# Kernel optimization log

Measured on AMD Instinct MI355X. Metric: run time of the kernel, lower is better.

## Reference

```python
import jax, jax.numpy as jnp
import numpy as np

TEMP_LP = 0.05  # args.temp_lp_loss


def setup_inputs() -> dict:
    key = jax.random.key(0)
    k1, k2, k3, k4 = jax.random.split(key, 4)
    B, B_s, topk, C, n_ids = 4096, 4096, 4, 128, 751
    feats = jax.random.normal(k1, (B, C), dtype=jnp.float32)
    feats_s = jax.random.normal(k2, (B_s, topk, C), dtype=jnp.float32)
    labels = jax.random.randint(k3, (B,), 0, n_ids)
    labels_s = jax.random.randint(k4, (B_s * topk,), 0, n_ids)
    return {"feats": feats, "feats_s": feats_s, "labels": labels, "labels_s": labels_s}


def reference(feats, feats_s, labels, labels_s):
    # feats: [B, C]; feats_s: [B_s, topk, C] -> [N, C] with N = B_s*topk
    B, C = feats.shape
    fs = feats_s.reshape(-1, C)
    sim = (feats @ fs.T) / TEMP_LP                      # [B, N]
    # Per-sample: target puts weight 1/P on the P positives (labels_s == label),
    # 0 on negatives. Concatenation order does not affect log_softmax values, so
    # loss_i = -(1/P) * sum_{j in pos} (sim[i,j] - logsumexp(sim[i,:]))
    lse = jax.nn.logsumexpsim = None
    lse = jax.nn.logsumexp(sim, axis=1)                 # [B]
    pos = labels[:, None] == labels_s[None, :]          # [B, N] bool
    P = pos.sum(axis=1).astype(sim.dtype)               # [B]
    pos_sum = jnp.sum(jnp.where(pos, sim, jnp.zeros((), sim.dtype)), axis=1)
    loss_i = lse - pos_sum / P                          # [B]
    return jnp.sum(loss_i) / B
```

## Files before the change

kernel.cpp:

```cpp
#include <hip/hip_runtime.h>
#include <hip/hip_bf16.h>

#define B_ROWS 4096
#define N_COLS 16384
#define CDIM   128
#define NIDS   751
#define TEMP_INV 20.0f
#define ASCALE 28.853900817779268f
#define LN2 0.6931471805599453f

#define BM 256
#define BN 64
#define NCHUNK 32
#define COLS_PER_CHUNK (N_COLS / NCHUNK)
#define STEPS (COLS_PER_CHUNK / BN)
#define LSE_BLOCKS ((B_ROWS / BM) * NCHUNK)
#define POS_BLOCKS (N_COLS / 256)

typedef __attribute__((ext_vector_type(8))) short short8;
typedef __attribute__((ext_vector_type(4))) float f32x4;
typedef __attribute__((ext_vector_type(4))) unsigned short u16x4;

#define AS1 __attribute__((address_space(1)))
#define AS3 __attribute__((address_space(3)))

__device__ __forceinline__ unsigned short f2bf(float x) {
  union { float f; unsigned u; } c; c.f = x;
  unsigned r = c.u + 0x7FFFu + ((c.u >> 16) & 1u);
  return (unsigned short)(r >> 16);
}

__global__ void prep_kernel(const float* __restrict__ feats, const float* __restrict__ fs,
                            const int* __restrict__ labels, const int* __restrict__ labels_s,
                            unsigned short* __restrict__ feats_bf, unsigned short* __restrict__ fs_bf,
                            float* __restrict__ Ftab, float* __restrict__ Pcnt) {
  const int bid = blockIdx.x;
  const int NF4 = B_ROWS * CDIM / 4;
  const int NCVT_BLK = (NF4 + N_COLS * CDIM / 4) / 256;
  if (bid < NCVT_BLK) {
    int idx = bid * 256 + threadIdx.x;
    if (idx < NF4) {
      f32x4 v = ((const f32x4*)feats)[idx];
      u16x4 o = { f2bf(v[0] * ASCALE), f2bf(v[1] * ASCALE), f2bf(v[2] * ASCALE), f2bf(v[3] * ASCALE) };
      ((u16x4*)feats_bf)[idx] = o;
    } else {
      int j = idx - NF4;
      f32x4 v = ((const f32x4*)fs)[j];
      u16x4 o = { f2bf(v[0]), f2bf(v[1]), f2bf(v[2]), f2bf(v[3]) };
      ((u16x4*)fs_bf)[j] = o;
    }
  } else if (bid < NCVT_BLK + (B_ROWS * CDIM) / 256) {
    int idx = (bid - NCVT_BLK) * 256 + threadIdx.x;
    int row = idx >> 7, c = idx & 127;
    atomicAdd(&Ftab[labels[row] * CDIM + c], feats[idx]);
  } else {
    int j = (bid - NCVT_BLK - (B_ROWS * CDIM) / 256) * 256 + threadIdx.x;
    atomicAdd(&Pcnt[labels_s[j]], 1.0f);
  }
}

__launch_bounds__(256, 2)
__global__ void main_kernel(const unsigned short* __restrict__ A,
                            const unsigned short* __restrict__ Bm,
                            const float* __restrict__ fs32,
                            const int* __restrict__ labels_s,
                            const float* __restrict__ Ftab, const float* __restrict__ Pcnt,
                            float* __restrict__ pm, float* __restrict__ ps,
                            float* __restrict__ acc) {
  __shared__ unsigned short lds[2][BN * CDIM];
  __shared__ float wsum[4];

  if (blockIdx.x >= LSE_BLOCKS) {
    int j = (blockIdx.x - LSE_BLOCKS) * 256 + threadIdx.x;
    int l = labels_s[j];
    const f32x4* fr = (const f32x4*)(fs32 + (size_t)j * CDIM);
    const f32x4* Fr = (const f32x4*)(Ftab + (size_t)l * CDIM);
    float d = 0.f;
#pragma unroll
    for (int q = 0; q < CDIM / 4; ++q) {
      f32x4 a = fr[q], b = Fr[q];
      d += a[0] * b[0] + a[1] * b[1] + a[2] * b[2] + a[3] * b[3];
    }
    d /= Pcnt[l];
#pragma unroll
    for (int off = 1; off < 64; off <<= 1) d += __shfl_xor(d, off, 64);
    if ((threadIdx.x & 63) == 0) wsum[threadIdx.x >> 6] = d;
    __syncthreads();
    if (threadIdx.x == 0) atomicAdd(&acc[1], wsum[0] + wsum[1] + wsum[2] + wsum[3]);
    return;
  }

  const int tid = threadIdx.x, wv = tid >> 6, ln = tid & 63;
  const int hi = ln >> 4, lo = ln & 15;
  const int ch = blockIdx.x & (NCHUNK - 1);
  const int rb = blockIdx.x >> 5;
  const int col_base = ch * COLS_PER_CHUNK;

  const unsigned short* aptr = A + (size_t)(rb * BM + wv * 64 + lo) * CDIM + hi * 8;
  short8 afr[4][4];
#pragma unroll
  for (int rg = 0; rg < 4; ++rg)
#pragma unroll
    for (int kk = 0; kk < 4; ++kk)
      afr[rg][kk] = *(const short8*)(aptr + rg * 16 * CDIM + kk * 32);

  float m_[4][4], s_[4][4];
#pragma unroll
  for (int rg = 0; rg < 4; ++rg)
#pragma unroll
    for (int j = 0; j < 4; ++j) { m_[rg][j] = -1e30f; s_[rg][j] = 0.f; }

  auto stage = [&](int buf, int step) {
    const int c0 = col_base + step * BN;
    char* base = (char*)&lds[buf][0];
#pragma unroll
    for (int r = 0; r < 4; ++r) {
      int q = r * 256 + wv * 64 + ln;
      int row = q >> 4, cc = q & 15;
      int cs = cc ^ (row & 7);
      const unsigned short* src = Bm + (size_t)(c0 + row) * CDIM + cs * 8;
      __builtin_amdgcn_global_load_lds((AS1 const void*)src,
                                       (AS3 void*)(base + (size_t)(r * 256 + wv * 64) * 16),
                                       16, 0, 0);
    }
  };

  stage(0, 0);
  int cur = 0;
  for (int t = 0; t < STEPS; ++t) {
    if (t + 1 < STEPS) {
      stage(cur ^ 1, t + 1);
      asm volatile("s_waitcnt vmcnt(4)" ::: "memory");
    } else {
      asm volatile("s_waitcnt vmcnt(0)" ::: "memory");
    }
    __builtin_amdgcn_s_barrier();
    __builtin_amdgcn_sched_barrier(0);

    f32x4 accv[4][4];
#pragma unroll
    for (int ct = 0; ct < 4; ++ct) {
      const int rowT = ct * 16 + lo;
      short8 bf[4];
#pragma unroll
      for (int kk = 0; kk < 4; ++kk) {
        int q = kk * 4 + hi;
        int qs = q ^ (rowT & 7);
        bf[kk] = *(const short8*)&lds[cur][rowT * CDIM + qs * 8];
      }
#pragma unroll
      for (int rg = 0; rg < 4; ++rg) {
        f32x4 c4 = {0.f, 0.f, 0.f, 0.f};
#pragma unroll
        for (int kk = 0; kk < 4; ++kk)
          c4 = __builtin_amdgcn_mfma_f32_16x16x32_bf16(afr[rg][kk], bf[kk], c4, 0, 0, 0);
        accv[rg][ct] = c4;
      }
    }

#pragma unroll
    for (int rg = 0; rg < 4; ++rg)
#pragma unroll
      for (int j = 0; j < 4; ++j) {
        float v0 = accv[rg][0][j], v1 = accv[rg][1][j];
        float v2 = accv[rg][2][j], v3 = accv[rg][3][j];
        float mx = fmaxf(fmaxf(v0, v1), fmaxf(v2, v3));
        float mn = fmaxf(m_[rg][j], mx);
        s_[rg][j] = s_[rg][j] * __builtin_amdgcn_exp2f(m_[rg][j] - mn)
                  + (__builtin_amdgcn_exp2f(v0 - mn) + __builtin_amdgcn_exp2f(v1 - mn))
                  + (__builtin_amdgcn_exp2f(v2 - mn) + __builtin_amdgcn_exp2f(v3 - mn));
        m_[rg][j] = mn;
      }

    __builtin_amdgcn_sched_barrier(0);
    __builtin_amdgcn_s_barrier();
    cur ^= 1;
  }

#pragma unroll
  for (int rg = 0; rg < 4; ++rg)
#pragma unroll
    for (int j = 0; j < 4; ++j) {
#pragma unroll
      for (int off = 1; off < 16; off <<= 1) {
        float mo = __shfl_xor(m_[rg][j], off, 64);
        float so = __shfl_xor(s_[rg][j], off, 64);
        float mn = fmaxf(m_[rg][j], mo);
        s_[rg][j] = s_[rg][j] * __builtin_amdgcn_exp2f(m_[rg][j] - mn)
                  + so * __builtin_amdgcn_exp2f(mo - mn);
        m_[rg][j] = mn;
      }
    }

  if (lo == 0) {
    int rbase = rb * BM + wv * 64;
#pragma unroll
    for (int rg = 0; rg < 4; ++rg)
#pragma unroll
      for (int j = 0; j < 4; ++j) {
        int row = rbase + rg * 16 + hi * 4 + j;
        pm[(size_t)ch * B_ROWS + row] = m_[rg][j];
        ps[(size_t)ch * B_ROWS + row] = s_[rg][j];
      }
  }
}

__global__ void combine_kernel(const float* __restrict__ pm, const float* __restrict__ ps,
                               float* __restrict__ acc, float* __restrict__ out) {
  int row = blockIdx.x * blockDim.x + threadIdx.x;
  float mg = -1e30f, sg = 0.f;
#pragma unroll
  for (int c = 0; c < NCHUNK; ++c) {
    float mp = pm[c * B_ROWS + row], sp = ps[c * B_ROWS + row];
    float mn = fmaxf(mg, mp);
    sg = sg * __builtin_amdgcn_exp2f(mg - mn) + sp * __builtin_amdgcn_exp2f(mp - mn);
    mg = mn;
  }
  float lse = LN2 * mg + logf(sg);
#pragma unroll
  for (int off = 1; off < 64; off <<= 1) lse += __shfl_xor(lse, off, 64);
  __shared__ float wsum[4];
  if ((threadIdx.x & 63) == 0) wsum[threadIdx.x >> 6] = lse;
  __syncthreads();
  if (threadIdx.x == 0) {
    atomicAdd(&acc[0], wsum[0] + wsum[1] + wsum[2] + wsum[3]);
    __threadfence();
    unsigned old = atomicAdd((unsigned*)&acc[2], 1u);
    if (old == (B_ROWS / 256) - 1) {
      float a0 = atomicAdd(&acc[0], 0.f);
      float a1 = atomicAdd(&acc[1], 0.f);
      out[0] = (a0 - TEMP_INV * a1) * (1.0f / (float)B_ROWS);
    }
  }
}

extern "C" void kernel_launch(void* const* d_in, const int* in_sizes, int n_in,
                              void* d_out, int out_size, void* d_ws, size_t ws_size,
                              hipStream_t stream) {
  const float* feats   = (const float*)d_in[0];
  const float* feats_s = (const float*)d_in[1];
  const int* labels    = (const int*)d_in[2];
  const int* labels_s  = (const int*)d_in[3];
  float* out = (float*)d_out;

  char* ws = (char*)d_ws;
  size_t off = 0;
  auto carve = [&](size_t bytes) -> char* {
    char* p = ws + off;
    off += (bytes + 255) & ~(size_t)255;
    return p;
  };
  unsigned short* feats_bf = (unsigned short*)carve((size_t)B_ROWS * CDIM * 2);
  unsigned short* fs_bf    = (unsigned short*)carve((size_t)N_COLS * CDIM * 2);
  size_t zstart = off;
  float* Ftab = (float*)carve((size_t)NIDS * CDIM * 4);
  float* Pcnt = (float*)carve((size_t)NIDS * 4);
  float* acc  = (float*)carve(4 * 4);
  size_t zend = off;
  float* pm   = (float*)carve((size_t)NCHUNK * B_ROWS * 4);
  float* ps   = (float*)carve((size_t)NCHUNK * B_ROWS * 4);

  hipMemsetAsync(ws + zstart, 0, zend - zstart, stream);

  const int NPREP = (B_ROWS * CDIM / 4 + N_COLS * CDIM / 4) / 256
                  + (B_ROWS * CDIM) / 256
                  + N_COLS / 256;
  prep_kernel<<<NPREP, 256, 0, stream>>>(feats, feats_s, labels, labels_s,
                                         feats_bf, fs_bf, Ftab, Pcnt);
  main_kernel<<<LSE_BLOCKS + POS_BLOCKS, 256, 0, stream>>>(feats_bf, fs_bf, feats_s, labels_s,
                                                           Ftab, Pcnt, pm, ps, acc);
  combine_kernel<<<B_ROWS / 256, 256, 0, stream>>>(pm, ps, acc, out);
}
```

Measured before the change: 112.7 us.

## Replace global-atomic scatter with per-label LDS tables, drop memset, fuse partial LSE

Class-sum and count tables are now built by per-16-label blocks that each scan the labels, gather matching rows into a shared list and accumulate them with shared-memory atomics. This replaces global float atomics and removes the separate memset launch, since the tables are fully written and acc is zeroed inside prep. The main kernel now writes a single log2-sum per chunk instead of separate max and sum arrays, which halves partial traffic and simplifies the combine. The LDS swizzle is widened to 16. The rewritten prep rescans all labels in every table block, and the list is capped at 2048 entries per 16 labels; a larger group would silently drop rows.

Measured after the change: 148.6 us. 31.9% more time.

```diff
diff --git a/kernel.cpp b/kernel.cpp
--- a/kernel.cpp
+++ b/kernel.cpp
@@ -16,6 +16,7 @@
 #define STEPS (COLS_PER_CHUNK / BN)
 #define LSE_BLOCKS ((B_ROWS / BM) * NCHUNK)
 #define POS_BLOCKS (N_COLS / 256)
+#define NTBL ((NIDS + 15) / 16)
 
 typedef __attribute__((ext_vector_type(8))) short short8;
 typedef __attribute__((ext_vector_type(4))) float f32x4;
@@ -33,12 +34,48 @@
 __global__ void prep_kernel(const float* __restrict__ feats, const float* __restrict__ fs,
                             const int* __restrict__ labels, const int* __restrict__ labels_s,
                             unsigned short* __restrict__ feats_bf, unsigned short* __restrict__ fs_bf,
-                            float* __restrict__ Ftab, float* __restrict__ Pcnt) {
+                            float* __restrict__ Ftab, float* __restrict__ Pcnt,
+                            float* __restrict__ acc) {
   const int bid = blockIdx.x;
-  const int NF4 = B_ROWS * CDIM / 4;
-  const int NCVT_BLK = (NF4 + N_COLS * CDIM / 4) / 256;
-  if (bid < NCVT_BLK) {
-    int idx = bid * 256 + threadIdx.x;
+  const int tid = threadIdx.x;
+  if (bid < NTBL) {
+    __shared__ float Facc[16 * CDIM];
+    __shared__ int   list[2048];
+    __shared__ float Pc[16];
+    __shared__ int   cnt;
+    const int lo_l = bid * 16;
+    if (bid == 0 && tid < 4) acc[tid] = 0.f;
+    for (int i = tid; i < 16 * CDIM; i += 256) Facc[i] = 0.f;
+    if (tid < 16) Pc[tid] = 0.f;
+    if (tid == 0) cnt = 0;
+    __syncthreads();
+    for (int r = tid; r < B_ROWS; r += 256) {
+      unsigned d = (unsigned)(labels[r] - lo_l);
+      if (d < 16u) {
+        int k = atomicAdd(&cnt, 1);
+        if (k < 2048) list[k] = (r << 4) | (int)d;
+      }
+    }
+    for (int r = tid; r < N_COLS; r += 256) {
+      unsigned d = (unsigned)(labels_s[r] - lo_l);
+      if (d < 16u) atomicAdd(&Pc[d], 1.0f);
+    }
+    __syncthreads();
+    int n = min(cnt, 2048);
+    int c = tid & 127;
+    for (int k = tid >> 7; k < n; k += 2) {
+      int e = list[k]; int r = e >> 4, ll = e & 15;
+      atomicAdd(&Facc[ll * CDIM + c], feats[(size_t)r * CDIM + c]);
+    }
+    __syncthreads();
+    for (int i = tid; i < 16 * CDIM; i += 256) {
+      int gl = lo_l + (i >> 7);
+      if (gl < NIDS) Ftab[(size_t)gl * CDIM + (i & 127)] = Facc[i];
+    }
+    if (tid < 16 && lo_l + tid < NIDS) Pcnt[lo_l + tid] = Pc[tid];
+  } else {
+    const int NF4 = B_ROWS * CDIM / 4;
+    int idx = (bid - NTBL) * 256 + tid;
     if (idx < NF4) {
       f32x4 v = ((const f32x4*)feats)[idx];
       u16x4 o = { f2bf(v[0] * ASCALE), f2bf(v[1] * ASCALE), f2bf(v[2] * ASCALE), f2bf(v[3] * ASCALE) };
@@ -49,13 +86,6 @@
       u16x4 o = { f2bf(v[0]), f2bf(v[1]), f2bf(v[2]), f2bf(v[3]) };
       ((u16x4*)fs_bf)[j] = o;
     }
-  } else if (bid < NCVT_BLK + (B_ROWS * CDIM) / 256) {
-    int idx = (bid - NCVT_BLK) * 256 + threadIdx.x;
-    int row = idx >> 7, c = idx & 127;
-    atomicAdd(&Ftab[labels[row] * CDIM + c], feats[idx]);
-  } else {
-    int j = (bid - NCVT_BLK - (B_ROWS * CDIM) / 256) * 256 + threadIdx.x;
-    atomicAdd(&Pcnt[labels_s[j]], 1.0f);
   }
 }
 
@@ -65,13 +95,14 @@
                             const float* __restrict__ fs32,
                             const int* __restrict__ labels_s,
                             const float* __restrict__ Ftab, const float* __restrict__ Pcnt,
-                            float* __restrict__ pm, float* __restrict__ ps,
+                            float* __restrict__ pmL,
                             float* __restrict__ acc) {
   __shared__ unsigned short lds[2][BN * CDIM];
   __shared__ float wsum[4];
+  const int tid = threadIdx.x;
 
   if (blockIdx.x >= LSE_BLOCKS) {
-    int j = (blockIdx.x - LSE_BLOCKS) * 256 + threadIdx.x;
+    int j = (blockIdx.x - LSE_BLOCKS) * 256 + tid;
     int l = labels_s[j];
     const f32x4* fr = (const f32x4*)(fs32 + (size_t)j * CDIM);
     const f32x4* Fr = (const f32x4*)(Ftab + (size_t)l * CDIM);
@@ -84,13 +115,13 @@
     d /= Pcnt[l];
 #pragma unroll
     for (int off = 1; off < 64; off <<= 1) d += __shfl_xor(d, off, 64);
-    if ((threadIdx.x & 63) == 0) wsum[threadIdx.x >> 6] = d;
-    __syncthreads();
-    if (threadIdx.x == 0) atomicAdd(&acc[1], wsum[0] + wsum[1] + wsum[2] + wsum[3]);
+    if ((tid & 63) == 0) wsum[tid >> 6] = d;
+    __syncthreads();
+    if (tid == 0) atomicAdd(&acc[1], wsum[0] + wsum[1] + wsum[2] + wsum[3]);
     return;
   }
 
-  const int tid = threadIdx.x, wv = tid >> 6, ln = tid & 63;
+  const int wv = tid >> 6, ln = tid & 63;
   const int hi = ln >> 4, lo = ln & 15;
   const int ch = blockIdx.x & (NCHUNK - 1);
   const int rb = blockIdx.x >> 5;
@@ -117,7 +148,7 @@
     for (int r = 0; r < 4; ++r) {
       int q = r * 256 + wv * 64 + ln;
       int row = q >> 4, cc = q & 15;
-      int cs = cc ^ (row & 7);
+      int cs = cc ^ (row & 15);
       const unsigned short* src = Bm + (size_t)(c0 + row) * CDIM + cs * 8;
       __builtin_amdgcn_global_load_lds((AS1 const void*)src,
                                        (AS3 void*)(base + (size_t)(r * 256 + wv * 64) * 16),
@@ -144,8 +175,7 @@
       short8 bf[4];
 #pragma unroll
       for (int kk = 0; kk < 4; ++kk) {
-        int q = kk * 4 + hi;
-        int qs = q ^ (rowT & 7);
+        int qs = (kk * 4 + hi) ^ (rowT & 15);
         bf[kk] = *(const short8*)&lds[cur][rowT * CDIM + qs * 8];
       }
 #pragma unroll
@@ -193,29 +223,31 @@
     }
 
   if (lo == 0) {
-    int rbase = rb * BM + wv * 64;
+    int rbase = rb * BM + wv * 64 + hi * 4;
 #pragma unroll
     for (int rg = 0; rg < 4; ++rg)
 #pragma unroll
       for (int j = 0; j < 4; ++j) {
-        int row = rbase + rg * 16 + hi * 4 + j;
-        pm[(size_t)ch * B_ROWS + row] = m_[rg][j];
-        ps[(size_t)ch * B_ROWS + row] = s_[rg][j];
-      }
-  }
-}
-
-__global__ void combine_kernel(const float* __restrict__ pm, const float* __restrict__ ps,
-                               float* __restrict__ acc, float* __restrict__ out) {
+        int row = rbase + rg * 16 + j;
+        pmL[(size_t)ch * B_ROWS + row] = m_[rg][j] + __log2f(s_[rg][j]);
+      }
+  }
+}
+
+__global__ void combine_kernel(const float* __restrict__ pmL,
+                               float* __restrict__ acc,
+                               float* __restrict__ out) {
   int row = blockIdx.x * blockDim.x + threadIdx.x;
-  float mg = -1e30f, sg = 0.f;
+  float L[NCHUNK];
+  float mg = -1e30f;
 #pragma unroll
   for (int c = 0; c < NCHUNK; ++c) {
-    float mp = pm[c * B_ROWS + row], sp = ps[c * B_ROWS + row];
-    float mn = fmaxf(mg, mp);
-    sg = sg * __builtin_amdgcn_exp2f(mg - mn) + sp * __builtin_amdgcn_exp2f(mp - mn);
-    mg = mn;
-  }
+    L[c] = pmL[c * B_ROWS + row];
+    mg = fmaxf(mg, L[c]);
+  }
+  float sg = 0.f;
+#pragma unroll
+  for (int c = 0; c < NCHUNK; ++c) sg += __builtin_amdgcn_exp2f(L[c] - mg);
   float lse = LN2 * mg + logf(sg);
 #pragma unroll
   for (int off = 1; off < 64; off <<= 1) lse += __shfl_xor(lse, off, 64);
@@ -252,22 +284,15 @@
   };
   unsigned short* feats_bf = (unsigned short*)carve((size_t)B_ROWS * CDIM * 2);
   unsigned short* fs_bf    = (unsigned short*)carve((size_t)N_COLS * CDIM * 2);
-  size_t zstart = off;
   float* Ftab = (float*)carve((size_t)NIDS * CDIM * 4);
   float* Pcnt = (float*)carve((size_t)NIDS * 4);
+  float* pmL  = (float*)carve((size_t)NCHUNK * B_ROWS * 4);
   float* acc  = (float*)carve(4 * 4);
-  size_t zend = off;
-  float* pm   = (float*)carve((size_t)NCHUNK * B_ROWS * 4);
-  float* ps   = (float*)carve((size_t)NCHUNK * B_ROWS * 4);
-
-  hipMemsetAsync(ws + zstart, 0, zend - zstart, stream);
-
-  const int NPREP = (B_ROWS * CDIM / 4 + N_COLS * CDIM / 4) / 256
-                  + (B_ROWS * CDIM) / 256
-                  + N_COLS / 256;
-  prep_kernel<<<NPREP, 256, 0, stream>>>(feats, feats_s, labels, labels_s,
-                                         feats_bf, fs_bf, Ftab, Pcnt);
+
+  const int NCVT = (B_ROWS * CDIM / 4 + N_COLS * CDIM / 4) / 256;
+  prep_kernel<<<NTBL + NCVT, 256, 0, stream>>>(feats, feats_s, labels, labels_s,
+                                               feats_bf, fs_bf, Ftab, Pcnt, acc);
   main_kernel<<<LSE_BLOCKS + POS_BLOCKS, 256, 0, stream>>>(feats_bf, fs_bf, feats_s, labels_s,
-                                                           Ftab, Pcnt, pm, ps, acc);
-  combine_kernel<<<B_ROWS / 256, 256, 0, stream>>>(pm, ps, acc, out);
-}
+                                                           Ftab, Pcnt, pmL, acc);
+  combine_kernel<<<B_ROWS / 256, 256, 0, stream>>>(pmL, acc, out);
+}
```
